# Kernel optimization log

Measured on AMD Instinct MI355X. Metric: run time of the kernel, lower is better.

## Reference

```python
import jax, jax.numpy as jnp
import numpy as np
from jax import lax

LATENT, HIDDEN, OUT = 64, 128, 64
B, T = 4096, 100


def setup_inputs() -> dict:
    key = jax.random.key(0)
    ks = jax.random.split(key, 12)
    s = lambda fan_in: 1.0 / np.sqrt(fan_in)
    u = lambda k, shape, fan_in: jax.random.uniform(k, shape, jnp.float32, -s(fan_in), s(fan_in))
    return {
        "z0": jax.random.normal(ks[0], (B, LATENT), jnp.float32),
        "t": jnp.arange(T, dtype=jnp.float32) * 0.01,  # increasing time grid
        "fc1_w": u(ks[1], (HIDDEN, LATENT), LATENT), "fc1_b": u(ks[2], (HIDDEN,), LATENT),
        "fc2_w": u(ks[3], (HIDDEN, HIDDEN), HIDDEN), "fc2_b": u(ks[4], (HIDDEN,), HIDDEN),
        "fc3_w": u(ks[5], (LATENT, HIDDEN), HIDDEN), "fc3_b": u(ks[6], (LATENT,), HIDDEN),
        "l2h_w": u(ks[7], (HIDDEN, LATENT), LATENT), "l2h_b": u(ks[8], (HIDDEN,), LATENT),
        "h2o_w": u(ks[9], (OUT, HIDDEN), HIDDEN), "h2o_b": u(ks[10], (OUT,), HIDDEN),
    }


def reference(z0, t, fc1_w, fc1_b, fc2_w, fc2_b, fc3_w, fc3_b, l2h_w, l2h_b, h2o_w, h2o_b):
    elu = jax.nn.elu

    def f(z):  # ODE_Func: fc1-elu-fc2-elu-fc3
        h = elu(z @ fc1_w.T + fc1_b)
        h = elu(h @ fc2_w.T + fc2_b)
        return h @ fc3_w.T + fc3_b

    dts = t[1:] - t[:-1]  # [T-1]

    def step(z, dt):  # fixed-step RK4
        k1 = f(z)
        k2 = f(z + 0.5 * dt * k1)
        k3 = f(z + 0.5 * dt * k2)
        k4 = f(z + dt * k3)
        zn = z + (dt / 6.0) * (k1 + 2.0 * k2 + 2.0 * k3 + k4)
        return zn, zn

    _, zs = lax.scan(step, z0, dts)          # [T-1, B, latent]
    pred_z = jnp.concatenate([z0[None], zs], axis=0)  # whole sequence [T, B, latent]
    # decode: h2o(relu(l2h(pred_z)))
    h = jax.nn.relu(pred_z @ l2h_w.T + l2h_b)
    return h @ h2o_w.T + h2o_b               # [T, B, out]
```

## Files before the change

### kernel.cpp

```cpp
#include <hip/hip_runtime.h>

typedef _Float16 f16;
typedef _Float16 f16x4 __attribute__((ext_vector_type(4)));
typedef _Float16 f16x8 __attribute__((ext_vector_type(8)));
typedef float    f32x4 __attribute__((ext_vector_type(4)));

#define MFMA16(a,b,c) __builtin_amdgcn_mfma_f32_16x16x32_f16((a),(b),(c),0,0,0)

#define LATENT 64
#define HIDDEN 128

__device__ __forceinline__ f16x8 load_afrag(const float* __restrict__ W, int K,
                                            int tile, int kf, int lane) {
  const int row = tile * 16 + (lane & 15);
  const int k0  = kf * 32 + (lane >> 4) * 8;
  const float* p = W + row * K + k0;
  f16x8 r;
#pragma unroll
  for (int j = 0; j < 8; ++j) r[j] = (f16)p[j];
  return r;
}

__device__ __forceinline__ f16x8 bfrag(const f16* buf, int rowb, int k0, int lane) {
  const int b  = lane & 15;
  const int kk = k0 + (lane >> 4) * 8;
  const int off = b * rowb + ((kk * 2) ^ ((b & 7) << 4));
  return *(const f16x8*)((const char*)buf + off);
}

__device__ __forceinline__ void dwrite(f16* buf, int rowb, int dbase, f32x4 v, int lane) {
  const int b = lane & 15;
  f16x4 h;
#pragma unroll
  for (int i = 0; i < 4; ++i) h[i] = (f16)v[i];
  const int off = b * rowb + ((dbase * 2) ^ ((b & 7) << 4));
  *(f16x4*)((char*)buf + off) = h;
}

__device__ __forceinline__ f32x4 elu4(f32x4 v) {
#pragma unroll
  for (int i = 0; i < 4; ++i) v[i] = v[i] > 0.f ? v[i] : (__expf(v[i]) - 1.f);
  return v;
}

__device__ __forceinline__ void bar_raw() {
  __builtin_amdgcn_s_barrier();
  __builtin_amdgcn_sched_barrier(0);
}

__global__ __launch_bounds__(512, 2)
void node_rk4_kernel(const float* __restrict__ z0,   const float* __restrict__ tg,
                     const float* __restrict__ fc1w, const float* __restrict__ fc1b,
                     const float* __restrict__ fc2w, const float* __restrict__ fc2b,
                     const float* __restrict__ fc3w, const float* __restrict__ fc3b,
                     const float* __restrict__ l2hw, const float* __restrict__ l2hb,
                     const float* __restrict__ h2ow, const float* __restrict__ h2ob,
                     float* __restrict__ out, int Btot, int T) {
  __shared__ __align__(16) f16 zhist[4][16 * 64];
  __shared__ __align__(16) f16 xbuf[16 * 64];
  __shared__ __align__(16) f16 h1buf[16 * 128];
  __shared__ __align__(16) f16 h2buf[16 * 128];
  __shared__ __align__(16) f16 dch1[16 * 128];

  const int tid  = threadIdx.x;
  const int lane = tid & 63;
  const int wv   = tid >> 6;
  const int iw   = wv & 3;
  const int grp  = lane >> 4;
  const int bcol = lane & 15;
  const int row0 = blockIdx.x * 16;

  if (wv < 4) {
    f16x8 a1[2][2], a2[2][4], a3[4];
    f32x4 b1[2], b2[2], b3;
#pragma unroll
    for (int ot = 0; ot < 2; ++ot) {
#pragma unroll
      for (int kf = 0; kf < 2; ++kf) a1[ot][kf] = load_afrag(fc1w, 64, 2 * iw + ot, kf, lane);
#pragma unroll
      for (int kf = 0; kf < 4; ++kf) a2[ot][kf] = load_afrag(fc2w, 128, 2 * iw + ot, kf, lane);
      const int d = (2 * iw + ot) * 16 + grp * 4;
      b1[ot] = *(const f32x4*)(fc1b + d);
      b2[ot] = *(const f32x4*)(fc2b + d);
    }
#pragma unroll
    for (int kf = 0; kf < 4; ++kf) a3[kf] = load_afrag(fc3w, 128, iw, kf, lane);
    const int dz = iw * 16 + grp * 4;
    b3 = *(const f32x4*)(fc3b + dz);

    f32x4 z = *(const f32x4*)(z0 + (size_t)(row0 + bcol) * LATENT + dz);

    auto feval = [&](const f16* xb) -> f32x4 {
      const f16x8 v0 = bfrag(xb, 128, 0, lane);
      const f16x8 v1 = bfrag(xb, 128, 32, lane);
#pragma unroll
      for (int ot = 0; ot < 2; ++ot) {
        f32x4 d = {0.f, 0.f, 0.f, 0.f};
        d = MFMA16(a1[ot][0], v0, d);
        d = MFMA16(a1[ot][1], v1, d);
        d += b1[ot];
        d = elu4(d);
        dwrite(h1buf, 256, (2 * iw + ot) * 16 + grp * 4, d, lane);
      }
      __syncthreads();
      f16x8 h[4];
#pragma unroll
      for (int kf = 0; kf < 4; ++kf) h[kf] = bfrag(h1buf, 256, kf * 32, lane);
#pragma unroll
      for (int ot = 0; ot < 2; ++ot) {
        f32x4 c0 = {0.f, 0.f, 0.f, 0.f}, c1 = {0.f, 0.f, 0.f, 0.f};
        c0 = MFMA16(a2[ot][0], h[0], c0);
        c0 = MFMA16(a2[ot][1], h[1], c0);
        c1 = MFMA16(a2[ot][2], h[2], c1);
        c1 = MFMA16(a2[ot][3], h[3], c1);
        f32x4 d = c0 + c1 + b2[ot];
        d = elu4(d);
        dwrite(h2buf, 256, (2 * iw + ot) * 16 + grp * 4, d, lane);
      }
      __syncthreads();
      f16x8 g[4];
#pragma unroll
      for (int kf = 0; kf < 4; ++kf) g[kf] = bfrag(h2buf, 256, kf * 32, lane);
      f32x4 c0 = {0.f, 0.f, 0.f, 0.f}, c1 = {0.f, 0.f, 0.f, 0.f};
      c0 = MFMA16(a3[0], g[0], c0);
      c0 = MFMA16(a3[1], g[1], c0);
      c1 = MFMA16(a3[2], g[2], c1);
      c1 = MFMA16(a3[3], g[3], c1);
      return c0 + c1 + b3;
    };

    for (int s = 0; s < T; ++s) {
      dwrite(zhist[s & 3], 128, dz, z, lane);
      __syncthreads();
      if (s == T - 1) break;
      const float dt = tg[s + 1] - tg[s];

      f32x4 k = feval(zhist[s & 3]);
      f32x4 acc = k, xs;
#pragma unroll
      for (int i = 0; i < 4; ++i) xs[i] = z[i] + 0.5f * dt * k[i];
      dwrite(xbuf, 128, dz, xs, lane);
      __syncthreads();
      k = feval(xbuf);
#pragma unroll
      for (int i = 0; i < 4; ++i) { acc[i] += 2.f * k[i]; xs[i] = z[i] + 0.5f * dt * k[i]; }
      dwrite(xbuf, 128, dz, xs, lane);
      __syncthreads();
      k = feval(xbuf);
#pragma unroll
      for (int i = 0; i < 4; ++i) { acc[i] += 2.f * k[i]; xs[i] = z[i] + dt * k[i]; }
      dwrite(xbuf, 128, dz, xs, lane);
      __syncthreads();
      k = feval(xbuf);
#pragma unroll
      for (int i = 0; i < 4; ++i) z[i] += (dt / 6.f) * (acc[i] + k[i]);
    }
  } else {
    f16x8 aL[8][2], aO[4][4];
    f32x4 bLr[8], bOr[4];
#pragma unroll
    for (int ot = 0; ot < 8; ++ot) {
      aL[ot][0] = load_afrag(l2hw, 64, ot, 0, lane);
      aL[ot][1] = load_afrag(l2hw, 64, ot, 1, lane);
      bLr[ot] = *(const f32x4*)(l2hb + ot * 16 + grp * 4);
    }
#pragma unroll
    for (int t = 0; t < 4; ++t) {
#pragma unroll
      for (int kf = 0; kf < 4; ++kf) aO[t][kf] = load_afrag(h2ow, 128, t, kf, lane);
      bOr[t] = *(const f32x4*)(h2ob + t * 16 + grp * 4);
    }

    for (int s = 0; s < T; ++s) {
      bar_raw();
      if ((s & 3) == iw) {
        const f16* zb = zhist[s & 3];
        const f16x8 zf0 = bfrag(zb, 128, 0, lane);
        const f16x8 zf1 = bfrag(zb, 128, 32, lane);
#pragma unroll
        for (int ot = 0; ot < 8; ++ot) {
          f32x4 d = {0.f, 0.f, 0.f, 0.f};
          d = MFMA16(aL[ot][0], zf0, d);
          d = MFMA16(aL[ot][1], zf1, d);
          d += bLr[ot];
#pragma unroll
          for (int i = 0; i < 4; ++i) d[i] = fmaxf(d[i], 0.f);
          dwrite(dch1, 256, ot * 16 + grp * 4, d, lane);
        }
        f16x8 h[4];
#pragma unroll
        for (int kf = 0; kf < 4; ++kf) h[kf] = bfrag(dch1, 256, kf * 32, lane);
#pragma unroll
        for (int t = 0; t < 4; ++t) {
          f32x4 c0 = {0.f, 0.f, 0.f, 0.f}, c1 = {0.f, 0.f, 0.f, 0.f};
          c0 = MFMA16(aO[t][0], h[0], c0);
          c0 = MFMA16(aO[t][1], h[1], c0);
          c1 = MFMA16(aO[t][2], h[2], c1);
          c1 = MFMA16(aO[t][3], h[3], c1);
          f32x4 o = c0 + c1 + bOr[t];
          *(f32x4*)(out + ((size_t)s * Btot + row0 + bcol) * LATENT + t * 16 + grp * 4) = o;
        }
      }
      if (s < T - 1) {
#pragma unroll 1
        for (int b2 = 0; b2 < 11; ++b2) bar_raw();
      }
    }
  }
}

extern "C" void kernel_launch(void* const* d_in, const int* in_sizes, int n_in,
                              void* d_out, int out_size, void* d_ws, size_t ws_size,
                              hipStream_t stream) {
  const float* z0   = (const float*)d_in[0];
  const float* tg   = (const float*)d_in[1];
  const float* fc1w = (const float*)d_in[2];
  const float* fc1b = (const float*)d_in[3];
  const float* fc2w = (const float*)d_in[4];
  const float* fc2b = (const float*)d_in[5];
  const float* fc3w = (const float*)d_in[6];
  const float* fc3b = (const float*)d_in[7];
  const float* l2hw = (const float*)d_in[8];
  const float* l2hb = (const float*)d_in[9];
  const float* h2ow = (const float*)d_in[10];
  const float* h2ob = (const float*)d_in[11];
  float* out = (float*)d_out;

  const int Btot = in_sizes[0] / LATENT;
  const int T    = in_sizes[1];

  dim3 grid(Btot / 16), block(512);
  node_rk4_kernel<<<grid, block, 0, stream>>>(z0, tg, fc1w, fc1b, fc2w, fc2b,
                                              fc3w, fc3b, l2hw, l2hb, h2ow, h2ob,
                                              out, Btot, T);
}
```

Before: 335.7 us.

## Split RK4 integration into single-wave blocks and a separate decode kernel

Replaces the 512-thread block (4 integrator waves plus 4 decoder waves synchronised through block barriers) with a 64-thread kernel where one wave holds all fc1/fc2/fc3 weights in registers and runs RK4 with no block barriers. The trajectory is written to the output buffer, then a second fully parallel kernel decodes each 16-row slab in place with l2h/h2o. This removes the barrier cost of every stage and decouples decoding from the serial loop. In exchange it adds a full write and read of the latent trajectory through global memory, uses heavy register pressure in one wave, and offers less latency hiding per CU.

New measurement: 1.002 ms. 199% more time.

```diff
diff --git a/kernel.cpp b/kernel.cpp
--- a/kernel.cpp
+++ b/kernel.cpp
@@ -37,175 +37,196 @@
   *(f16x4*)((char*)buf + off) = h;
 }
 
-__device__ __forceinline__ f32x4 elu4(f32x4 v) {
-#pragma unroll
-  for (int i = 0; i < 4; ++i) v[i] = v[i] > 0.f ? v[i] : (__expf(v[i]) - 1.f);
-  return v;
-}
-
-__device__ __forceinline__ void bar_raw() {
-  __builtin_amdgcn_s_barrier();
-  __builtin_amdgcn_sched_barrier(0);
-}
-
-__global__ __launch_bounds__(512, 2)
-void node_rk4_kernel(const float* __restrict__ z0,   const float* __restrict__ tg,
-                     const float* __restrict__ fc1w, const float* __restrict__ fc1b,
-                     const float* __restrict__ fc2w, const float* __restrict__ fc2b,
-                     const float* __restrict__ fc3w, const float* __restrict__ fc3b,
-                     const float* __restrict__ l2hw, const float* __restrict__ l2hb,
-                     const float* __restrict__ h2ow, const float* __restrict__ h2ob,
-                     float* __restrict__ out, int Btot, int T) {
-  __shared__ __align__(16) f16 zhist[4][16 * 64];
-  __shared__ __align__(16) f16 xbuf[16 * 64];
-  __shared__ __align__(16) f16 h1buf[16 * 128];
-  __shared__ __align__(16) f16 h2buf[16 * 128];
-  __shared__ __align__(16) f16 dch1[16 * 128];
+__device__ __forceinline__ f32x4 elu4(f32x4 d) {
+#pragma unroll
+  for (int i = 0; i < 4; ++i) {
+    const float e = __expf(d[i]) - 1.f;
+    d[i] = d[i] > 0.f ? d[i] : e;
+  }
+  return d;
+}
+
+__global__ __launch_bounds__(64, 1)
+void node_int(const float* __restrict__ z0,   const float* __restrict__ tg,
+              const float* __restrict__ fc1w, const float* __restrict__ fc1b,
+              const float* __restrict__ fc2w, const float* __restrict__ fc2b,
+              const float* __restrict__ fc3w, const float* __restrict__ fc3b,
+              float* __restrict__ out, int Btot, int T) {
+  __shared__ __align__(16) f16 xb[16 * 64];
+  __shared__ __align__(16) f16 h1[16 * 128];
+  __shared__ __align__(16) f16 h2[16 * 128];
+
+  const int lane = threadIdx.x;
+  const int grp  = lane >> 4;
+  const int bcol = lane & 15;
+  const int row0 = blockIdx.x * 16;
+  const f32x4 Z0 = {0.f, 0.f, 0.f, 0.f};
+
+  f16x8 a1[8][2], a2[8][4], a3[4][4];
+  f32x4 b1[8], b2[8], b3[4];
+#pragma unroll
+  for (int ot = 0; ot < 8; ++ot) {
+    a1[ot][0] = load_afrag(fc1w, 64, ot, 0, lane);
+    a1[ot][1] = load_afrag(fc1w, 64, ot, 1, lane);
+#pragma unroll
+    for (int kf = 0; kf < 4; ++kf) a2[ot][kf] = load_afrag(fc2w, 128, ot, kf, lane);
+    b1[ot] = *(const f32x4*)(fc1b + ot * 16 + grp * 4);
+    b2[ot] = *(const f32x4*)(fc2b + ot * 16 + grp * 4);
+  }
+#pragma unroll
+  for (int ot = 0; ot < 4; ++ot) {
+#pragma unroll
+    for (int kf = 0; kf < 4; ++kf) a3[ot][kf] = load_afrag(fc3w, 128, ot, kf, lane);
+    b3[ot] = *(const f32x4*)(fc3b + ot * 16 + grp * 4);
+  }
+
+  f32x4 z[4];
+#pragma unroll
+  for (int zt = 0; zt < 4; ++zt)
+    z[zt] = *(const f32x4*)(z0 + (size_t)(row0 + bcol) * LATENT + zt * 16 + grp * 4);
+
+  auto feval = [&](const f32x4 x[4], f32x4 k[4]) {
+#pragma unroll
+    for (int zt = 0; zt < 4; ++zt) dwrite(xb, 128, zt * 16 + grp * 4, x[zt], lane);
+    const f16x8 v0 = bfrag(xb, 128, 0, lane);
+    const f16x8 v1 = bfrag(xb, 128, 32, lane);
+#pragma unroll
+    for (int ot = 0; ot < 8; ++ot) {
+      f32x4 d = MFMA16(a1[ot][0], v0, b1[ot]);
+      d = MFMA16(a1[ot][1], v1, d);
+      d = elu4(d);
+      dwrite(h1, 256, ot * 16 + grp * 4, d, lane);
+    }
+    f16x8 h[4];
+#pragma unroll
+    for (int kf = 0; kf < 4; ++kf) h[kf] = bfrag(h1, 256, kf * 32, lane);
+#pragma unroll
+    for (int ot = 0; ot < 8; ++ot) {
+      f32x4 c0 = MFMA16(a2[ot][0], h[0], b2[ot]);
+      c0 = MFMA16(a2[ot][1], h[1], c0);
+      f32x4 c1 = MFMA16(a2[ot][2], h[2], Z0);
+      c1 = MFMA16(a2[ot][3], h[3], c1);
+      f32x4 d = elu4(c0 + c1);
+      dwrite(h2, 256, ot * 16 + grp * 4, d, lane);
+    }
+    f16x8 g[4];
+#pragma unroll
+    for (int kf = 0; kf < 4; ++kf) g[kf] = bfrag(h2, 256, kf * 32, lane);
+#pragma unroll
+    for (int ot = 0; ot < 4; ++ot) {
+      f32x4 c0 = MFMA16(a3[ot][0], g[0], b3[ot]);
+      c0 = MFMA16(a3[ot][1], g[1], c0);
+      f32x4 c1 = MFMA16(a3[ot][2], g[2], Z0);
+      c1 = MFMA16(a3[ot][3], g[3], c1);
+      k[ot] = c0 + c1;
+    }
+  };
+
+  float t_cur = tg[0];
+  float t_nxt = tg[1];
+  for (int s = 0; s < T; ++s) {
+#pragma unroll
+    for (int zt = 0; zt < 4; ++zt)
+      *(f32x4*)(out + ((size_t)s * Btot + row0 + bcol) * LATENT + zt * 16 + grp * 4) = z[zt];
+    if (s == T - 1) break;
+
+    const float t_fut = tg[s + 2 < T ? s + 2 : T - 1];
+    const float dt = t_nxt - t_cur;
+
+    f32x4 k[4], acc[4], xs[4];
+    feval(z, k);
+#pragma unroll
+    for (int zt = 0; zt < 4; ++zt) {
+      acc[zt] = k[zt];
+#pragma unroll
+      for (int i = 0; i < 4; ++i) xs[zt][i] = z[zt][i] + 0.5f * dt * k[zt][i];
+    }
+    feval(xs, k);
+#pragma unroll
+    for (int zt = 0; zt < 4; ++zt)
+#pragma unroll
+      for (int i = 0; i < 4; ++i) {
+        acc[zt][i] += 2.f * k[zt][i];
+        xs[zt][i] = z[zt][i] + 0.5f * dt * k[zt][i];
+      }
+    feval(xs, k);
+#pragma unroll
+    for (int zt = 0; zt < 4; ++zt)
+#pragma unroll
+      for (int i = 0; i < 4; ++i) {
+        acc[zt][i] += 2.f * k[zt][i];
+        xs[zt][i] = z[zt][i] + dt * k[zt][i];
+      }
+    feval(xs, k);
+#pragma unroll
+    for (int zt = 0; zt < 4; ++zt)
+#pragma unroll
+      for (int i = 0; i < 4; ++i) z[zt][i] += (dt / 6.f) * (acc[zt][i] + k[zt][i]);
+
+    t_cur = t_nxt;
+    t_nxt = t_fut;
+  }
+}
+
+__global__ __launch_bounds__(256, 1)
+void node_dec(const float* __restrict__ l2hw, const float* __restrict__ l2hb,
+              const float* __restrict__ h2ow, const float* __restrict__ h2ob,
+              float* __restrict__ out) {
+  __shared__ __align__(16) f16 xb[4][16 * 64];
+  __shared__ __align__(16) f16 hb[4][16 * 128];
 
   const int tid  = threadIdx.x;
   const int lane = tid & 63;
   const int wv   = tid >> 6;
-  const int iw   = wv & 3;
   const int grp  = lane >> 4;
   const int bcol = lane & 15;
-  const int row0 = blockIdx.x * 16;
-
-  if (wv < 4) {
-    f16x8 a1[2][2], a2[2][4], a3[4];
-    f32x4 b1[2], b2[2], b3;
-#pragma unroll
-    for (int ot = 0; ot < 2; ++ot) {
-#pragma unroll
-      for (int kf = 0; kf < 2; ++kf) a1[ot][kf] = load_afrag(fc1w, 64, 2 * iw + ot, kf, lane);
-#pragma unroll
-      for (int kf = 0; kf < 4; ++kf) a2[ot][kf] = load_afrag(fc2w, 128, 2 * iw + ot, kf, lane);
-      const int d = (2 * iw + ot) * 16 + grp * 4;
-      b1[ot] = *(const f32x4*)(fc1b + d);
-      b2[ot] = *(const f32x4*)(fc2b + d);
-    }
-#pragma unroll
-    for (int kf = 0; kf < 4; ++kf) a3[kf] = load_afrag(fc3w, 128, iw, kf, lane);
-    const int dz = iw * 16 + grp * 4;
-    b3 = *(const f32x4*)(fc3b + dz);
-
-    f32x4 z = *(const f32x4*)(z0 + (size_t)(row0 + bcol) * LATENT + dz);
-
-    auto feval = [&](const f16* xb) -> f32x4 {
-      const f16x8 v0 = bfrag(xb, 128, 0, lane);
-      const f16x8 v1 = bfrag(xb, 128, 32, lane);
-#pragma unroll
-      for (int ot = 0; ot < 2; ++ot) {
-        f32x4 d = {0.f, 0.f, 0.f, 0.f};
-        d = MFMA16(a1[ot][0], v0, d);
-        d = MFMA16(a1[ot][1], v1, d);
-        d += b1[ot];
-        d = elu4(d);
-        dwrite(h1buf, 256, (2 * iw + ot) * 16 + grp * 4, d, lane);
-      }
-      __syncthreads();
-      f16x8 h[4];
-#pragma unroll
-      for (int kf = 0; kf < 4; ++kf) h[kf] = bfrag(h1buf, 256, kf * 32, lane);
-#pragma unroll
-      for (int ot = 0; ot < 2; ++ot) {
-        f32x4 c0 = {0.f, 0.f, 0.f, 0.f}, c1 = {0.f, 0.f, 0.f, 0.f};
-        c0 = MFMA16(a2[ot][0], h[0], c0);
-        c0 = MFMA16(a2[ot][1], h[1], c0);
-        c1 = MFMA16(a2[ot][2], h[2], c1);
-        c1 = MFMA16(a2[ot][3], h[3], c1);
-        f32x4 d = c0 + c1 + b2[ot];
-        d = elu4(d);
-        dwrite(h2buf, 256, (2 * iw + ot) * 16 + grp * 4, d, lane);
-      }
-      __syncthreads();
-      f16x8 g[4];
-#pragma unroll
-      for (int kf = 0; kf < 4; ++kf) g[kf] = bfrag(h2buf, 256, kf * 32, lane);
-      f32x4 c0 = {0.f, 0.f, 0.f, 0.f}, c1 = {0.f, 0.f, 0.f, 0.f};
-      c0 = MFMA16(a3[0], g[0], c0);
-      c0 = MFMA16(a3[1], g[1], c0);
-      c1 = MFMA16(a3[2], g[2], c1);
-      c1 = MFMA16(a3[3], g[3], c1);
-      return c0 + c1 + b3;
-    };
-
-    for (int s = 0; s < T; ++s) {
-      dwrite(zhist[s & 3], 128, dz, z, lane);
-      __syncthreads();
-      if (s == T - 1) break;
-      const float dt = tg[s + 1] - tg[s];
-
-      f32x4 k = feval(zhist[s & 3]);
-      f32x4 acc = k, xs;
-#pragma unroll
-      for (int i = 0; i < 4; ++i) xs[i] = z[i] + 0.5f * dt * k[i];
-      dwrite(xbuf, 128, dz, xs, lane);
-      __syncthreads();
-      k = feval(xbuf);
-#pragma unroll
-      for (int i = 0; i < 4; ++i) { acc[i] += 2.f * k[i]; xs[i] = z[i] + 0.5f * dt * k[i]; }
-      dwrite(xbuf, 128, dz, xs, lane);
-      __syncthreads();
-      k = feval(xbuf);
-#pragma unroll
-      for (int i = 0; i < 4; ++i) { acc[i] += 2.f * k[i]; xs[i] = z[i] + dt * k[i]; }
-      dwrite(xbuf, 128, dz, xs, lane);
-      __syncthreads();
-      k = feval(xbuf);
-#pragma unroll
-      for (int i = 0; i < 4; ++i) z[i] += (dt / 6.f) * (acc[i] + k[i]);
-    }
-  } else {
-    f16x8 aL[8][2], aO[4][4];
-    f32x4 bLr[8], bOr[4];
-#pragma unroll
-    for (int ot = 0; ot < 8; ++ot) {
-      aL[ot][0] = load_afrag(l2hw, 64, ot, 0, lane);
-      aL[ot][1] = load_afrag(l2hw, 64, ot, 1, lane);
-      bLr[ot] = *(const f32x4*)(l2hb + ot * 16 + grp * 4);
-    }
-#pragma unroll
-    for (int t = 0; t < 4; ++t) {
-#pragma unroll
-      for (int kf = 0; kf < 4; ++kf) aO[t][kf] = load_afrag(h2ow, 128, t, kf, lane);
-      bOr[t] = *(const f32x4*)(h2ob + t * 16 + grp * 4);
-    }
-
-    for (int s = 0; s < T; ++s) {
-      bar_raw();
-      if ((s & 3) == iw) {
-        const f16* zb = zhist[s & 3];
-        const f16x8 zf0 = bfrag(zb, 128, 0, lane);
-        const f16x8 zf1 = bfrag(zb, 128, 32, lane);
-#pragma unroll
-        for (int ot = 0; ot < 8; ++ot) {
-          f32x4 d = {0.f, 0.f, 0.f, 0.f};
-          d = MFMA16(aL[ot][0], zf0, d);
-          d = MFMA16(aL[ot][1], zf1, d);
-          d += bLr[ot];
-#pragma unroll
-          for (int i = 0; i < 4; ++i) d[i] = fmaxf(d[i], 0.f);
-          dwrite(dch1, 256, ot * 16 + grp * 4, d, lane);
-        }
-        f16x8 h[4];
-#pragma unroll
-        for (int kf = 0; kf < 4; ++kf) h[kf] = bfrag(dch1, 256, kf * 32, lane);
-#pragma unroll
-        for (int t = 0; t < 4; ++t) {
-          f32x4 c0 = {0.f, 0.f, 0.f, 0.f}, c1 = {0.f, 0.f, 0.f, 0.f};
-          c0 = MFMA16(aO[t][0], h[0], c0);
-          c0 = MFMA16(aO[t][1], h[1], c0);
-          c1 = MFMA16(aO[t][2], h[2], c1);
-          c1 = MFMA16(aO[t][3], h[3], c1);
-          f32x4 o = c0 + c1 + bOr[t];
-          *(f32x4*)(out + ((size_t)s * Btot + row0 + bcol) * LATENT + t * 16 + grp * 4) = o;
-        }
-      }
-      if (s < T - 1) {
-#pragma unroll 1
-        for (int b2 = 0; b2 < 11; ++b2) bar_raw();
-      }
-    }
+  const int r0   = (blockIdx.x * 4 + wv) * 16;
+  const f32x4 Z0 = {0.f, 0.f, 0.f, 0.f};
+
+  f16x8 aL[8][2], aO[4][4];
+  f32x4 bL[8], bO[4];
+#pragma unroll
+  for (int ot = 0; ot < 8; ++ot) {
+    aL[ot][0] = load_afrag(l2hw, 64, ot, 0, lane);
+    aL[ot][1] = load_afrag(l2hw, 64, ot, 1, lane);
+    bL[ot] = *(const f32x4*)(l2hb + ot * 16 + grp * 4);
+  }
+#pragma unroll
+  for (int t = 0; t < 4; ++t) {
+#pragma unroll
+    for (int kf = 0; kf < 4; ++kf) aO[t][kf] = load_afrag(h2ow, 128, t, kf, lane);
+    bO[t] = *(const f32x4*)(h2ob + t * 16 + grp * 4);
+  }
+
+  f32x4 zr[4];
+#pragma unroll
+  for (int ot = 0; ot < 4; ++ot) {
+    zr[ot] = *(const f32x4*)(out + (size_t)(r0 + bcol) * LATENT + ot * 16 + grp * 4);
+  }
+#pragma unroll
+  for (int ot = 0; ot < 4; ++ot) dwrite(xb[wv], 128, ot * 16 + grp * 4, zr[ot], lane);
+
+  const f16x8 v0 = bfrag(xb[wv], 128, 0, lane);
+  const f16x8 v1 = bfrag(xb[wv], 128, 32, lane);
+#pragma unroll
+  for (int ot = 0; ot < 8; ++ot) {
+    f32x4 d = MFMA16(aL[ot][0], v0, bL[ot]);
+    d = MFMA16(aL[ot][1], v1, d);
+#pragma unroll
+    for (int i = 0; i < 4; ++i) d[i] = fmaxf(d[i], 0.f);
+    dwrite(hb[wv], 256, ot * 16 + grp * 4, d, lane);
+  }
+  f16x8 h[4];
+#pragma unroll
+  for (int kf = 0; kf < 4; ++kf) h[kf] = bfrag(hb[wv], 256, kf * 32, lane);
+#pragma unroll
+  for (int t = 0; t < 4; ++t) {
+    f32x4 c0 = MFMA16(aO[t][0], h[0], bO[t]);
+    c0 = MFMA16(aO[t][1], h[1], c0);
+    f32x4 c1 = MFMA16(aO[t][2], h[2], Z0);
+    c1 = MFMA16(aO[t][3], h[3], c1);
+    f32x4 o = c0 + c1;
+    *(f32x4*)(out + (size_t)(r0 + bcol) * LATENT + t * 16 + grp * 4) = o;
   }
 }
 
@@ -229,8 +250,8 @@
   const int Btot = in_sizes[0] / LATENT;
   const int T    = in_sizes[1];
 
-  dim3 grid(Btot / 16), block(512);
-  node_rk4_kernel<<<grid, block, 0, stream>>>(z0, tg, fc1w, fc1b, fc2w, fc2b,
-                                              fc3w, fc3b, l2hw, l2hb, h2ow, h2ob,
-                                              out, Btot, T);
-}
+  node_int<<<dim3(Btot / 16), dim3(64), 0, stream>>>(z0, tg, fc1w, fc1b, fc2w, fc2b,
+                                                     fc3w, fc3b, out, Btot, T);
+  const int slabs = (T * Btot) / 16;
+  node_dec<<<dim3(slabs / 4), dim3(256), 0, stream>>>(l2hw, l2hb, h2ow, h2ob, out);
+}
```
